# Performance work log

Hardware: AMD Instinct MI355X
Metric: run time of the kernel (lower is better)

## Reference

```python
import jax, jax.numpy as jnp
import numpy as np

B, T, E, H = 4, 2048, 1024, 16
HD = E // H  # head dim = 64

def setup_inputs() -> dict:
    key = jax.random.key(0)
    ks = jax.random.split(key, 5)
    s = 1.0 / np.sqrt(E)
    return {
        "x": jax.random.normal(ks[0], (B, T, E), dtype=jnp.float32),
        "W_attn": jax.random.uniform(ks[1], (E, 3 * E), dtype=jnp.float32, minval=-s, maxval=s),
        "b_attn": jax.random.uniform(ks[2], (3 * E,), dtype=jnp.float32, minval=-s, maxval=s),
        "W_proj": jax.random.uniform(ks[3], (E, E), dtype=jnp.float32, minval=-s, maxval=s),
        "b_proj": jax.random.uniform(ks[4], (E,), dtype=jnp.float32, minval=-s, maxval=s),
    }

def reference(x, W_attn, b_attn, W_proj, b_proj):
    b, t, e = x.shape
    qkv = x @ W_attn + b_attn                      # [B,T,3E]
    q, k, v = jnp.split(qkv, 3, axis=-1)
    # [B,T,E] -> [B,H,T,HD]
    q = q.reshape(b, t, H, HD).transpose(0, 2, 1, 3)
    k = k.reshape(b, t, H, HD).transpose(0, 2, 1, 3)
    v = v.reshape(b, t, H, HD).transpose(0, 2, 1, 3)
    att = jnp.einsum('bhqd,bhkd->bhqk', q, k) * (1.0 / np.sqrt(HD))
    causal_mask = jnp.tril(jnp.ones((t, t), dtype=bool))
    att = jnp.where(causal_mask[None, None, :, :], att, -jnp.inf)
    att = jax.nn.softmax(att, axis=-1)             # drop=0 -> dropout is identity
    y = jnp.einsum('bhqk,bhkd->bhqd', att, v)      # [B,H,T,HD]
    y = y.transpose(0, 2, 1, 3).reshape(b, t, e)
    return y @ W_proj + b_proj
```

## Files before the change

### kernel.cpp

```cpp
#include <hip/hip_runtime.h>
#include <hip/hip_bf16.h>
#include <stdint.h>


#define B_  4
#define T_  2048
#define E_  1024
#define H_  16
#define HD_ 64

typedef unsigned short u16;
typedef __bf16 bf16x8 __attribute__((ext_vector_type(8)));
typedef float f32x4 __attribute__((ext_vector_type(4)));
typedef float f32x16 __attribute__((ext_vector_type(16)));
typedef unsigned uint2v __attribute__((ext_vector_type(2)));

struct alignas(8) us4 { u16 x, y, z, w; };

__device__ __forceinline__ u16 tobf(float f) {
  union { __bf16 h; u16 u; } c;
  c.h = (__bf16)f;
  return c.u;
}

__device__ __forceinline__ void gload_lds16(const void* g, void* l) {
  auto gp = reinterpret_cast<const __attribute__((address_space(1))) uint32_t*>(
      reinterpret_cast<uintptr_t>(g));
  auto lp = reinterpret_cast<__attribute__((address_space(3))) uint32_t*>(
      reinterpret_cast<uintptr_t>(l));
  __builtin_amdgcn_global_load_lds(gp, lp, 16, 0, 0);
}

__device__ __forceinline__ bf16x8 ld_frag(const u16* p) {
  return *reinterpret_cast<const bf16x8*>(p);
}

#define BARRIER() do { __builtin_amdgcn_s_barrier(); asm volatile("" ::: "memory"); } while (0)
#define LDS_BARRIER() do { \
  asm volatile("s_waitcnt lgkmcnt(0)" ::: "memory"); \
  __builtin_amdgcn_s_barrier(); \
  asm volatile("" ::: "memory"); \
} while (0)


__global__ void prep_kernel(const float* __restrict__ x, u16* __restrict__ xb,
                            const float* __restrict__ Wa, u16* __restrict__ waT,
                            const float* __restrict__ Wp, u16* __restrict__ wpT) {
  __shared__ u16 tile[32][33];
  const int bid = blockIdx.x;
  if (bid < 8192) {
    const int i = (bid * 256 + threadIdx.x) * 4;
    float4 v = *reinterpret_cast<const float4*>(x + i);
    us4 o = { tobf(v.x), tobf(v.y), tobf(v.z), tobf(v.w) };
    *reinterpret_cast<us4*>(xb + i) = o;
  } else {
    const int idx = bid - 8192;
    const int bx = idx & 127, by = idx >> 7;
    const float* in;
    u16* out;
    int N, n0;
    if (bx < 96) { in = Wa; out = waT; N = 3072; n0 = bx * 32; }
    else         { in = Wp; out = wpT; N = 1024; n0 = (bx - 96) * 32; }
    const int k0 = by * 32;
    const int tx = threadIdx.x & 31, ty = threadIdx.x >> 5;
#pragma unroll
    for (int i = 0; i < 32; i += 8)
      tile[ty + i][tx] = tobf(in[(size_t)(k0 + ty + i) * N + n0 + tx]);
    __syncthreads();
#pragma unroll
    for (int i = 0; i < 32; i += 8)
      out[(size_t)(n0 + ty + i) * 1024 + k0 + tx] = tile[tx][ty + i];
  }
}


template <int MODE>
__launch_bounds__(512, 2)
__global__ void gemm_kernel(const u16* __restrict__ A, const u16* __restrict__ Bt,
                            const float* __restrict__ bias,
                            u16* __restrict__ qws, u16* __restrict__ kws,
                            u16* __restrict__ vtws, float* __restrict__ out) {
  constexpr int K = 1024, NT = 16;
  __shared__ u16 Asm[3 * 8192];
  __shared__ u16 Bsm[3 * 16384];
  const int tid = threadIdx.x;
  const int wid = tid >> 6, lane = tid & 63;
  const int wm = wid >> 2, wn = wid & 3;
  const int row0 = blockIdx.x * 128, col0 = blockIdx.y * 256;

  const int sgrow = wid * 8 + (lane >> 3);
  const int sgslot = (lane & 7) ^ (lane >> 3);
  const int lrow = lane & 15, lks = lane >> 4, r7 = lrow & 7;
  const int ca0 = ((lks) ^ r7) * 8;
  const int ca1 = ((4 + lks) ^ r7) * 8;
  const int bhalf = (wn >> 1) * 8192 + (wn & 1) * 4096;

#define STG_A(sb, kt, j)                                                        \
  gload_lds16(A + (size_t)(row0 + (j) * 64 + sgrow) * K + (kt) * 64 + sgslot * 8, \
              &Asm[(sb) * 8192 + (j) * 4096 + wid * 512])
#define STG_B(sb, kt, h, j)                                                     \
  gload_lds16(Bt + (size_t)(col0 + (h) * 128 + (j) * 64 + sgrow) * K + (kt) * 64 + sgslot * 8, \
              &Bsm[(sb) * 16384 + (h) * 8192 + (j) * 4096 + wid * 512])
#define RDA(mi, cc) ld_frag(&Asm[rb * 8192 + (wm * 64 + (mi) * 16 + lrow) * 64 + (cc)])
#define RDB(ni, cc) ld_frag(&Bsm[rb * 16384 + bhalf + ((ni) * 16 + lrow) * 64 + (cc)])

  f32x4 acc[4][4] = {};

  STG_A(0, 0, 0); STG_A(0, 0, 1);
  STG_B(0, 0, 0, 0); STG_B(0, 0, 0, 1); STG_B(0, 0, 1, 0); STG_B(0, 0, 1, 1);
  STG_A(1, 1, 0); STG_A(1, 1, 1);
  STG_B(1, 1, 0, 0); STG_B(1, 1, 0, 1); STG_B(1, 1, 1, 0); STG_B(1, 1, 1, 1);
  asm volatile("s_waitcnt vmcnt(6)" ::: "memory");
  BARRIER();

  for (int t = 0; t < NT; ++t) {
    const int rb = t % 3;
    const int sb = (t + 2) % 3;
    const bool hs = (t + 2) < NT;
    const int kt = t + 2;
    bf16x8 af[4], bf[4];

    af[0] = RDA(0, ca0); af[1] = RDA(1, ca0); af[2] = RDA(2, ca0); af[3] = RDA(3, ca0);
    bf[0] = RDB(0, ca0); bf[1] = RDB(1, ca0); bf[2] = RDB(2, ca0); bf[3] = RDB(3, ca0);
    if (hs) { STG_A(sb, kt, 0); STG_A(sb, kt, 1); }
    __builtin_amdgcn_s_setprio(1);
#pragma unroll
    for (int mi = 0; mi < 4; ++mi)
#pragma unroll
      for (int ni = 0; ni < 4; ++ni)
        acc[mi][ni] = __builtin_amdgcn_mfma_f32_16x16x32_bf16(af[mi], bf[ni], acc[mi][ni], 0, 0, 0);
    __builtin_amdgcn_s_setprio(0);

    af[0] = RDA(0, ca1); af[1] = RDA(1, ca1); af[2] = RDA(2, ca1); af[3] = RDA(3, ca1);
    bf[0] = RDB(0, ca1); bf[1] = RDB(1, ca1); bf[2] = RDB(2, ca1); bf[3] = RDB(3, ca1);
    if (hs) { STG_B(sb, kt, 0, 0); STG_B(sb, kt, 0, 1); STG_B(sb, kt, 1, 0); STG_B(sb, kt, 1, 1); }
    __builtin_amdgcn_s_setprio(1);
#pragma unroll
    for (int mi = 0; mi < 4; ++mi)
#pragma unroll
      for (int ni = 0; ni < 4; ++ni)
        acc[mi][ni] = __builtin_amdgcn_mfma_f32_16x16x32_bf16(af[mi], bf[ni], acc[mi][ni], 0, 0, 0);
    __builtin_amdgcn_s_setprio(0);

    if (hs) asm volatile("s_waitcnt vmcnt(6)" ::: "memory");
    else    asm volatile("s_waitcnt vmcnt(0)" ::: "memory");
    BARRIER();
  }
#undef STG_A
#undef STG_B
#undef RDA
#undef RDB

  if constexpr (MODE == 0) {
    const int part = (col0 + wn * 64) >> 10;
    if (part < 2) {
#pragma unroll
      for (int mi = 0; mi < 4; ++mi) {
#pragma unroll
        for (int ni = 0; ni < 4; ++ni) {
          const int gr0 = row0 + wm * 64 + mi * 16 + (lane >> 4) * 4;
          const int gc = col0 + wn * 64 + ni * 16 + (lane & 15);
          const float bv = bias[gc];
          const int e = gc & 1023;
          const int h = e >> 6, d = e & 63;
#pragma unroll
          for (int r = 0; r < 4; ++r) {
            const int m = gr0 + r;
            const int b = m >> 11, tt = m & 2047;
            const float val = acc[mi][ni][r] + bv;
            const size_t bh = (size_t)(b * H_ + h);
            if (part == 0)
              qws[(bh * T_ + tt) * HD_ + d] = tobf(val * 0.1803368801f);
            else
              kws[(bh * T_ + tt) * HD_ + d] = tobf(val);
          }
        }
      }
    } else {
      u16* vt_l = &Bsm[wid * 4608];
#pragma unroll
      for (int mi = 0; mi < 4; ++mi)
#pragma unroll
        for (int ni = 0; ni < 4; ++ni) {
          const float bv = bias[col0 + wn * 64 + ni * 16 + (lane & 15)];
#pragma unroll
          for (int r = 0; r < 4; ++r)
            vt_l[(ni * 16 + (lane & 15)) * 72 + mi * 16 + (lane >> 4) * 4 + r] =
                tobf(acc[mi][ni][r] + bv);
        }
      const int e0 = col0 + wn * 64 - 2048;
      const int h = e0 >> 6;
      const int m0 = row0 + wm * 64;
      const int b = m0 >> 11, tbase = m0 & 2047;
      u16* vbase = vtws + (size_t)(b * H_ + h) * HD_ * T_;
#pragma unroll
      for (int it = 0; it < 8; ++it) {
        const int d = it * 8 + (lane >> 3);
        const uint4 vv = *reinterpret_cast<const uint4*>(&vt_l[d * 72 + (lane & 7) * 8]);
        *reinterpret_cast<uint4*>(&vbase[(size_t)d * T_ + tbase + (lane & 7) * 8]) = vv;
      }
    }
  } else {
#pragma unroll
    for (int mi = 0; mi < 4; ++mi) {
#pragma unroll
      for (int ni = 0; ni < 4; ++ni) {
        const int gr0 = row0 + wm * 64 + mi * 16 + (lane >> 4) * 4;
        const int gc = col0 + wn * 64 + ni * 16 + (lane & 15);
        const float bv = bias[gc];
#pragma unroll
        for (int r = 0; r < 4; ++r)
          out[(size_t)(gr0 + r) * E_ + gc] = acc[mi][ni][r] + bv;
      }
    }
  }
}


__launch_bounds__(256, 4)
__global__ void attn_kernel(const u16* __restrict__ q, const u16* __restrict__ k,
                            const u16* __restrict__ vt, u16* __restrict__ y) {
  __shared__ u16 kl[2][64 * 68];
  __shared__ u16 vl[2][64 * 68];
  const int tid = threadIdx.x, w = tid >> 6, lane = tid & 63;
  const int l31 = lane & 31, hi = lane >> 5;
  const int bid = blockIdx.x;
  const int p = (bid >> 6) & 15;
  const int bh = bid & 63;
  const u16* qp = q + (size_t)bh * T_ * HD_;
  const u16* kp = k + (size_t)bh * T_ * HD_;
  const u16* vp = vt + (size_t)bh * HD_ * T_;
  const int b = bh >> 4, h = bh & 15;
  u16* yb = y + (size_t)b * T_ * E_ + h * HD_;

  const int unit = (w < 2) ? (31 - p) : p;
  const int qbw = unit * 64 + (w & 1) * 32;
  const int npass = 32 - p;

  bf16x8 aq[4];
#pragma unroll
  for (int slot = 0; slot < 4; ++slot)
    aq[slot] = ld_frag(qp + (size_t)(qbw + l31) * HD_ + slot * 16 + hi * 8);

  bf16x8 vone;
#pragma unroll
  for (int i = 0; i < 8; ++i) vone[i] = (__bf16)1.0f;

  f32x16 o0 = {}, o1 = {};
  f32x16 ls = {};

  const int srow = w * 8 + (lane >> 3);
  const int scol = (lane & 7) * 8;

  uint4 kreg[2], vreg[2];
#pragma unroll
  for (int c = 0; c < 2; ++c) {
    kreg[c] = *(const uint4*)(kp + (size_t)(c * 32 + srow) * HD_ + scol);
    vreg[c] = *(const uint4*)(vp + (size_t)(c * 32 + srow) * T_ + scol);
  }

  int buf = 0;
  for (int pass = 0; pass < npass; ++pass) {
    const int kv0 = pass * 64;
#pragma unroll
    for (int c = 0; c < 2; ++c) {
      const int row = c * 32 + srow;
      u16* kd = &kl[buf][row * 68 + scol];
      uint2 k0 = {kreg[c].x, kreg[c].y}, k1 = {kreg[c].z, kreg[c].w};
      *(uint2*)kd = k0;
      *(uint2*)(kd + 4) = k1;
      u16* vd = &vl[buf][row * 68 + scol];
      uint2 v0 = {vreg[c].x, vreg[c].y}, v1 = {vreg[c].z, vreg[c].w};
      *(uint2*)vd = v0;
      *(uint2*)(vd + 4) = v1;
    }
    if (pass + 1 < npass) {
      const int kvn = kv0 + 64;
#pragma unroll
      for (int c = 0; c < 2; ++c) {
        kreg[c] = *(const uint4*)(kp + (size_t)(kvn + c * 32 + srow) * HD_ + scol);
        vreg[c] = *(const uint4*)(vp + (size_t)(c * 32 + srow) * T_ + kvn + scol);
      }
    }
    LDS_BARRIER();

#pragma unroll
    for (int half = 0; half < 2; ++half) {
      const int kvh = kv0 + half * 32;
      if (kvh > qbw + 31) break;
      const int base = half * 32;

      f32x16 s = {};
      __builtin_amdgcn_s_setprio(1);
#pragma unroll
      for (int slot = 0; slot < 4; ++slot) {
        union { uint2 d[2]; bf16x8 v; } kf;
        const u16* kr = &kl[buf][(base + l31) * 68 + slot * 16 + hi * 8];
        kf.d[0] = *(const uint2*)kr;
        kf.d[1] = *(const uint2*)(kr + 4);
        s = __builtin_amdgcn_mfma_f32_32x32x16_bf16(kf.v, aq[slot], s, 0, 0, 0);
      }
      __builtin_amdgcn_s_setprio(0);

      if (kvh + 31 > qbw) {
        const int qq = qbw + l31;
#pragma unroll
        for (int r = 0; r < 16; ++r) {
          const int kv = kvh + (r & 3) + 8 * (r >> 2) + 4 * hi;
          if (kv > qq) s[r] = -1e30f;
        }
      }

#pragma unroll
      for (int r = 0; r < 16; ++r) s[r] = exp2f(s[r]);

      unsigned cw[8];
#pragma unroll
      for (int i = 0; i < 8; ++i) {
        union { __bf16 hh[2]; unsigned u; } pk;
        pk.hh[0] = (__bf16)s[2 * i];
        pk.hh[1] = (__bf16)s[2 * i + 1];
        cw[i] = pk.u;
      }
      union PU { unsigned u[4]; bf16x8 v; } pa0, pa1;
      {
        const uint2v q0 = __builtin_amdgcn_permlane32_swap(cw[0], cw[2], false, false);
        const uint2v q1 = __builtin_amdgcn_permlane32_swap(cw[1], cw[3], false, false);
        const uint2v q2 = __builtin_amdgcn_permlane32_swap(cw[4], cw[6], false, false);
        const uint2v q3 = __builtin_amdgcn_permlane32_swap(cw[5], cw[7], false, false);
        pa0.u[0] = q0.x; pa0.u[2] = q0.y;
        pa0.u[1] = q1.x; pa0.u[3] = q1.y;
        pa1.u[0] = q2.x; pa1.u[2] = q2.y;
        pa1.u[1] = q3.x; pa1.u[3] = q3.y;
      }

      __builtin_amdgcn_s_setprio(1);
      {
        union { uint2 d[2]; bf16x8 v; } vf;
        const u16* vr0 = &vl[buf][l31 * 68 + base + hi * 8];
        vf.d[0] = *(const uint2*)vr0;
        vf.d[1] = *(const uint2*)(vr0 + 4);
        o0 = __builtin_amdgcn_mfma_f32_32x32x16_bf16(pa0.v, vf.v, o0, 0, 0, 0);
        ls = __builtin_amdgcn_mfma_f32_32x32x16_bf16(pa0.v, vone, ls, 0, 0, 0);
        vf.d[0] = *(const uint2*)(vr0 + 16);
        vf.d[1] = *(const uint2*)(vr0 + 20);
        o0 = __builtin_amdgcn_mfma_f32_32x32x16_bf16(pa1.v, vf.v, o0, 0, 0, 0);
        ls = __builtin_amdgcn_mfma_f32_32x32x16_bf16(pa1.v, vone, ls, 0, 0, 0);
        const u16* vr1 = &vl[buf][(32 + l31) * 68 + base + hi * 8];
        vf.d[0] = *(const uint2*)vr1;
        vf.d[1] = *(const uint2*)(vr1 + 4);
        o1 = __builtin_amdgcn_mfma_f32_32x32x16_bf16(pa0.v, vf.v, o1, 0, 0, 0);
        vf.d[0] = *(const uint2*)(vr1 + 16);
        vf.d[1] = *(const uint2*)(vr1 + 20);
        o1 = __builtin_amdgcn_mfma_f32_32x32x16_bf16(pa1.v, vf.v, o1, 0, 0, 0);
      }
      __builtin_amdgcn_s_setprio(0);
    }
    buf ^= 1;
  }

#pragma unroll
  for (int r = 0; r < 16; ++r) {
    const int cr = (r & 3) + 8 * (r >> 2) + 4 * hi;
    const float li = 1.f / ls[r];
    const size_t row = (size_t)(qbw + cr) * E_;
    yb[row + l31] = tobf(o0[r] * li);
    yb[row + 32 + l31] = tobf(o1[r] * li);
  }
}


extern "C" void kernel_launch(void* const* d_in, const int* in_sizes, int n_in,
                              void* d_out, int out_size, void* d_ws, size_t ws_size,
                              hipStream_t stream) {
  const float* x  = (const float*)d_in[0];
  const float* Wa = (const float*)d_in[1];
  const float* ba = (const float*)d_in[2];
  const float* Wp = (const float*)d_in[3];
  const float* bp = (const float*)d_in[4];
  float* out = (float*)d_out;

  u16* ws   = (u16*)d_ws;
  u16* xb   = ws;
  u16* waT  = xb  + (size_t)8 * 1024 * 1024;
  u16* wpT  = waT + (size_t)3 * 1024 * 1024;
  u16* qws  = wpT + (size_t)1024 * 1024;
  u16* kws  = qws + (size_t)8 * 1024 * 1024;
  u16* vtws = kws + (size_t)8 * 1024 * 1024;
  u16* yws  = xb;

  prep_kernel<<<dim3(12288), dim3(256), 0, stream>>>(x, xb, Wa, waT, Wp, wpT);

  gemm_kernel<0><<<dim3(64, 12), dim3(512), 0, stream>>>(xb, waT, ba, qws, kws, vtws, nullptr);
  attn_kernel<<<dim3(1024), dim3(256), 0, stream>>>(qws, kws, vtws, yws);
  gemm_kernel<1><<<dim3(64, 4), dim3(512), 0, stream>>>(yws, wpT, bp, nullptr, nullptr, nullptr, out);
}
```

Measured before the change: 183.3 us.

## Pair two causal query tiles per wave to share K/V LDS fragment loads

Each wave now handles two 32-row query tiles (tA and its mirror 63-tA), so the K and V fragments read from shared memory once per 32-key step feed both tiles' QK and PV MFMAs. Pairing the mirrored tiles also balances causal work across blocks. The grid is halved to 512 blocks and launch bounds are relaxed to 2 blocks per SM, so more registers are available for the doubled accumulators and hoisted fragments. The risk is lower occupancy and fewer blocks to hide latency, and all four waves in a block now step through a shared kv pass count even where one tile has finished.

Measured after the change: 169.9 us. 1.08x faster.

```diff
diff --git a/kernel.cpp b/kernel.cpp
--- a/kernel.cpp
+++ b/kernel.cpp
@@ -217,7 +217,7 @@
 }
 
 
-__launch_bounds__(256, 4)
+__launch_bounds__(256, 2)
 __global__ void attn_kernel(const u16* __restrict__ q, const u16* __restrict__ k,
                             const u16* __restrict__ vt, u16* __restrict__ y) {
   __shared__ u16 kl[2][64 * 68];
@@ -225,7 +225,7 @@
   const int tid = threadIdx.x, w = tid >> 6, lane = tid & 63;
   const int l31 = lane & 31, hi = lane >> 5;
   const int bid = blockIdx.x;
-  const int p = (bid >> 6) & 15;
+  const int g = bid >> 6;
   const int bh = bid & 63;
   const u16* qp = q + (size_t)bh * T_ * HD_;
   const u16* kp = k + (size_t)bh * T_ * HD_;
@@ -233,21 +233,24 @@
   const int b = bh >> 4, h = bh & 15;
   u16* yb = y + (size_t)b * T_ * E_ + h * HD_;
 
-  const int unit = (w < 2) ? (31 - p) : p;
-  const int qbw = unit * 64 + (w & 1) * 32;
-  const int npass = 32 - p;
-
-  bf16x8 aq[4];
-#pragma unroll
-  for (int slot = 0; slot < 4; ++slot)
-    aq[slot] = ld_frag(qp + (size_t)(qbw + l31) * HD_ + slot * 16 + hi * 8);
+  const int tA = g * 4 + w;
+  const int tB = 63 - tA;
+  const int qbwA = tA * 32, qbwB = tB * 32;
+  const int npass = (64 - g * 4) >> 1;
+
+  bf16x8 aqA[4], aqB[4];
+#pragma unroll
+  for (int slot = 0; slot < 4; ++slot) {
+    aqA[slot] = ld_frag(qp + (size_t)(qbwA + l31) * HD_ + slot * 16 + hi * 8);
+    aqB[slot] = ld_frag(qp + (size_t)(qbwB + l31) * HD_ + slot * 16 + hi * 8);
+  }
 
   bf16x8 vone;
 #pragma unroll
   for (int i = 0; i < 8; ++i) vone[i] = (__bf16)1.0f;
 
-  f32x16 o0 = {}, o1 = {};
-  f32x16 ls = {};
+  f32x16 oA0 = {}, oA1 = {}, lsA = {};
+  f32x16 oB0 = {}, oB1 = {}, lsB = {};
 
   const int srow = w * 8 + (lane >> 3);
   const int scol = (lane & 7) * 8;
@@ -287,74 +290,85 @@
 #pragma unroll
     for (int half = 0; half < 2; ++half) {
       const int kvh = kv0 + half * 32;
-      if (kvh > qbw + 31) break;
+      const int kt = kvh >> 5;
+      const bool actA = kt <= tA;
+      const bool actB = kt <= tB;
+      if (!actB) break;
       const int base = half * 32;
 
-      f32x16 s = {};
-      __builtin_amdgcn_s_setprio(1);
+      union KV { uint2 d[2]; bf16x8 v; };
+      KV kf[4], vf0, vf1, vf2, vf3;
 #pragma unroll
       for (int slot = 0; slot < 4; ++slot) {
-        union { uint2 d[2]; bf16x8 v; } kf;
         const u16* kr = &kl[buf][(base + l31) * 68 + slot * 16 + hi * 8];
-        kf.d[0] = *(const uint2*)kr;
-        kf.d[1] = *(const uint2*)(kr + 4);
-        s = __builtin_amdgcn_mfma_f32_32x32x16_bf16(kf.v, aq[slot], s, 0, 0, 0);
-      }
-      __builtin_amdgcn_s_setprio(0);
-
-      if (kvh + 31 > qbw) {
-        const int qq = qbw + l31;
-#pragma unroll
-        for (int r = 0; r < 16; ++r) {
-          const int kv = kvh + (r & 3) + 8 * (r >> 2) + 4 * hi;
-          if (kv > qq) s[r] = -1e30f;
+        kf[slot].d[0] = *(const uint2*)kr;
+        kf[slot].d[1] = *(const uint2*)(kr + 4);
+      }
+      {
+        const u16* vr0 = &vl[buf][l31 * 68 + base + hi * 8];
+        vf0.d[0] = *(const uint2*)vr0;
+        vf0.d[1] = *(const uint2*)(vr0 + 4);
+        vf1.d[0] = *(const uint2*)(vr0 + 16);
+        vf1.d[1] = *(const uint2*)(vr0 + 20);
+        const u16* vr1 = &vl[buf][(32 + l31) * 68 + base + hi * 8];
+        vf2.d[0] = *(const uint2*)vr1;
+        vf2.d[1] = *(const uint2*)(vr1 + 4);
+        vf3.d[0] = *(const uint2*)(vr1 + 16);
+        vf3.d[1] = *(const uint2*)(vr1 + 20);
+      }
+
+      auto tile_round = [&](const bf16x8* aq, f32x16& o0, f32x16& o1,
+                            f32x16& ls, const int qbw) {
+        f32x16 s = {};
+        __builtin_amdgcn_s_setprio(1);
+#pragma unroll
+        for (int slot = 0; slot < 4; ++slot)
+          s = __builtin_amdgcn_mfma_f32_32x32x16_bf16(kf[slot].v, aq[slot], s, 0, 0, 0);
+        __builtin_amdgcn_s_setprio(0);
+
+        if (kvh + 31 > qbw) {
+          const int qq = qbw + l31;
+#pragma unroll
+          for (int r = 0; r < 16; ++r) {
+            const int kv = kvh + (r & 3) + 8 * (r >> 2) + 4 * hi;
+            if (kv > qq) s[r] = -1e30f;
+          }
         }
-      }
-
-#pragma unroll
-      for (int r = 0; r < 16; ++r) s[r] = exp2f(s[r]);
-
-      unsigned cw[8];
-#pragma unroll
-      for (int i = 0; i < 8; ++i) {
-        union { __bf16 hh[2]; unsigned u; } pk;
-        pk.hh[0] = (__bf16)s[2 * i];
-        pk.hh[1] = (__bf16)s[2 * i + 1];
-        cw[i] = pk.u;
-      }
-      union PU { unsigned u[4]; bf16x8 v; } pa0, pa1;
-      {
-        const uint2v q0 = __builtin_amdgcn_permlane32_swap(cw[0], cw[2], false, false);
-        const uint2v q1 = __builtin_amdgcn_permlane32_swap(cw[1], cw[3], false, false);
-        const uint2v q2 = __builtin_amdgcn_permlane32_swap(cw[4], cw[6], false, false);
-        const uint2v q3 = __builtin_amdgcn_permlane32_swap(cw[5], cw[7], false, false);
-        pa0.u[0] = q0.x; pa0.u[2] = q0.y;
-        pa0.u[1] = q1.x; pa0.u[3] = q1.y;
-        pa1.u[0] = q2.x; pa1.u[2] = q2.y;
-        pa1.u[1] = q3.x; pa1.u[3] = q3.y;
-      }
-
-      __builtin_amdgcn_s_setprio(1);
-      {
-        union { uint2 d[2]; bf16x8 v; } vf;
-        const u16* vr0 = &vl[buf][l31 * 68 + base + hi * 8];
-        vf.d[0] = *(const uint2*)vr0;
-        vf.d[1] = *(const uint2*)(vr0 + 4);
-        o0 = __builtin_amdgcn_mfma_f32_32x32x16_bf16(pa0.v, vf.v, o0, 0, 0, 0);
+#pragma unroll
+        for (int r = 0; r < 16; ++r) s[r] = exp2f(s[r]);
+
+        unsigned cw[8];
+#pragma unroll
+        for (int i = 0; i < 8; ++i) {
+          union { __bf16 hh[2]; unsigned u; } pk;
+          pk.hh[0] = (__bf16)s[2 * i];
+          pk.hh[1] = (__bf16)s[2 * i + 1];
+          cw[i] = pk.u;
+        }
+        union PU { unsigned u[4]; bf16x8 v; } pa0, pa1;
+        {
+          const uint2v q0 = __builtin_amdgcn_permlane32_swap(cw[0], cw[2], false, false);
+          const uint2v q1 = __builtin_amdgcn_permlane32_swap(cw[1], cw[3], false, false);
+          const uint2v q2 = __builtin_amdgcn_permlane32_swap(cw[4], cw[6], false, false);
+          const uint2v q3 = __builtin_amdgcn_permlane32_swap(cw[5], cw[7], false, false);
+          pa0.u[0] = q0.x; pa0.u[2] = q0.y;
+          pa0.u[1] = q1.x; pa0.u[3] = q1.y;
+          pa1.u[0] = q2.x; pa1.u[2] = q2.y;
+          pa1.u[1] = q3.x; pa1.u[3] = q3.y;
+        }
+
+        __builtin_amdgcn_s_setprio(1);
+        o0 = __builtin_amdgcn_mfma_f32_32x32x16_bf16(pa0.v, vf0.v, o0, 0, 0, 0);
         ls = __builtin_amdgcn_mfma_f32_32x32x16_bf16(pa0.v, vone, ls, 0, 0, 0);
-        vf.d[0] = *(const uint2*)(vr0 + 16);
-        vf.d[1] = *(const uint2*)(vr0 + 20);
-        o0 = __builtin_amdgcn_mfma_f32_32x32x16_bf16(pa1.v, vf.v, o0, 0, 0, 0);
+        o0 = __builtin_amdgcn_mfma_f32_32x32x16_bf16(pa1.v, vf1.v, o0, 0, 0, 0);
         ls = __builtin_amdgcn_mfma_f32_32x32x16_bf16(pa1.v, vone, ls, 0, 0, 0);
-        const u16* vr1 = &vl[buf][(32 + l31) * 68 + base + hi * 8];
-        vf.d[0] = *(const uint2*)vr1;
-        vf.d[1] = *(const uint2*)(vr1 + 4);
-        o1 = __builtin_amdgcn_mfma_f32_32x32x16_bf16(pa0.v, vf.v, o1, 0, 0, 0);
-        vf.d[0] = *(const uint2*)(vr1 + 16);
-        vf.d[1] = *(const uint2*)(vr1 + 20);
-        o1 = __builtin_amdgcn_mfma_f32_32x32x16_bf16(pa1.v, vf.v, o1, 0, 0, 0);
-      }
-      __builtin_amdgcn_s_setprio(0);
+        o1 = __builtin_amdgcn_mfma_f32_32x32x16_bf16(pa0.v, vf2.v, o1, 0, 0, 0);
+        o1 = __builtin_amdgcn_mfma_f32_32x32x16_bf16(pa1.v, vf3.v, o1, 0, 0, 0);
+        __builtin_amdgcn_s_setprio(0);
+      };
+
+      if (actA) tile_round(aqA, oA0, oA1, lsA, qbwA);
+      tile_round(aqB, oB0, oB1, lsB, qbwB);
     }
     buf ^= 1;
   }
@@ -362,10 +376,14 @@
 #pragma unroll
   for (int r = 0; r < 16; ++r) {
     const int cr = (r & 3) + 8 * (r >> 2) + 4 * hi;
-    const float li = 1.f / ls[r];
-    const size_t row = (size_t)(qbw + cr) * E_;
-    yb[row + l31] = tobf(o0[r] * li);
-    yb[row + 32 + l31] = tobf(o1[r] * li);
+    const float liA = 1.f / lsA[r];
+    const size_t rowA = (size_t)(qbwA + cr) * E_;
+    yb[rowA + l31] = tobf(oA0[r] * liA);
+    yb[rowA + 32 + l31] = tobf(oA1[r] * liA);
+    const float liB = 1.f / lsB[r];
+    const size_t rowB = (size_t)(qbwB + cr) * E_;
+    yb[rowB + l31] = tobf(oB0[r] * liB);
+    yb[rowB + 32 + l31] = tobf(oB1[r] * liB);
   }
 }
 
@@ -392,6 +410,6 @@
   prep_kernel<<<dim3(12288), dim3(256), 0, stream>>>(x, xb, Wa, waT, Wp, wpT);
 
   gemm_kernel<0><<<dim3(64, 12), dim3(512), 0, stream>>>(xb, waT, ba, qws, kws, vtws, nullptr);
-  attn_kernel<<<dim3(1024), dim3(256), 0, stream>>>(qws, kws, vtws, yws);
+  attn_kernel<<<dim3(512), dim3(256), 0, stream>>>(qws, kws, vtws, yws);
   gemm_kernel<1><<<dim3(64, 4), dim3(512), 0, stream>>>(yws, wpT, bp, nullptr, nullptr, nullptr, out);
 }
```
